# Kernel tuning notes

Hardware: AMD Instinct MI355X
Metric: run time of the kernel (lower is better)

## Reference

```python
import jax, jax.numpy as jnp
import numpy as np

HIDDEN = 1024
ATTN = 512


def setup_inputs() -> dict:
    key = jax.random.key(0)
    ks = jax.random.split(key, 7)
    B, S = 8, 2048
    inputs = jax.random.normal(ks[0], (B, S, HIDDEN), dtype=jnp.float32)
    s = 1.0 / np.sqrt(HIDDEN)
    Wq = jax.random.uniform(ks[1], (HIDDEN, ATTN), jnp.float32, -s, s)
    bq = jax.random.uniform(ks[2], (ATTN,), jnp.float32, -s, s)
    Wk = jax.random.uniform(ks[3], (HIDDEN, ATTN), jnp.float32, -s, s)
    bk = jax.random.uniform(ks[4], (ATTN,), jnp.float32, -s, s)
    Wv = jax.random.uniform(ks[5], (HIDDEN, ATTN), jnp.float32, -s, s)
    bv = jax.random.uniform(ks[6], (ATTN,), jnp.float32, -s, s)
    return {"inputs": inputs, "Wq": Wq, "bq": bq, "Wk": Wk, "bk": bk, "Wv": Wv, "bv": bv}


def reference(inputs, Wq, bq, Wk, bk, Wv, bv):
    # tanh-gated Q/K/V projections
    q = jnp.tanh(inputs @ Wq + bq)        # [B, S, A]
    k = jnp.tanh(inputs @ Wk + bk)        # [B, S, A]
    v = jnp.tanh(inputs @ Wv + bv)        # [B, S, A]
    scores = jnp.einsum('bqa,bka->bqk', q, k) / jnp.sqrt(jnp.float32(ATTN))
    probs = jax.nn.softmax(scores, axis=-1)   # [B, S, S]
    context = jnp.einsum('bqk,bka->bqa', probs, v)
    return jnp.tanh(context), probs
```

## Files before the change

kernel.cpp:

```cpp
#include <hip/hip_runtime.h>
#include <hip/hip_fp16.h>
#include <cstdint>

#define HIDDEN 1024
#define ATTN   512
#define NB     8
#define SEQ    2048
#define MROWS  (NB*SEQ)

typedef _Float16 f16x8 __attribute__((ext_vector_type(8)));
typedef _Float16 f16x4 __attribute__((ext_vector_type(4)));
typedef float    f32x4 __attribute__((ext_vector_type(4)));


__device__ __forceinline__ float tanh_fast(float x){
  float e = __expf(2.0f*x);
  return 1.0f - 2.0f/(e + 1.0f);
}

__device__ __forceinline__ void gload16(const void* g, void* l){
  __builtin_amdgcn_global_load_lds((const __attribute__((address_space(1))) void*)g,
                                   (__attribute__((address_space(3))) void*)l, 16, 0, 0);
}

__global__ __launch_bounds__(256) void k_cast_x(const float* __restrict__ x, __half* __restrict__ xh){
  size_t i = (size_t)blockIdx.x*256 + threadIdx.x;
  const float4* src = reinterpret_cast<const float4*>(x) + i*2;
  float4 a = src[0], b = src[1];
  f16x8 h;
  h[0]=(_Float16)a.x; h[1]=(_Float16)a.y; h[2]=(_Float16)a.z; h[3]=(_Float16)a.w;
  h[4]=(_Float16)b.x; h[5]=(_Float16)b.y; h[6]=(_Float16)b.z; h[7]=(_Float16)b.w;
  reinterpret_cast<f16x8*>(xh)[i] = h;
}

__global__ __launch_bounds__(256) void k_transpose_w(const float* __restrict__ Wq, const float* __restrict__ Wk,
                                                     const float* __restrict__ Wv, __half* __restrict__ whT){
  __shared__ float lds[32][33];
  int which = blockIdx.y;
  const float* W = which==0 ? Wq : (which==1 ? Wk : Wv);
  int tr = blockIdx.x >> 4;
  int tc = blockIdx.x & 15;
  int t = threadIdx.x;
  {
    int r = t >> 3, c4 = (t & 7)*4;
    float4 v = *reinterpret_cast<const float4*>(W + (size_t)(tr*32 + r)*ATTN + tc*32 + c4);
    lds[r][c4+0]=v.x; lds[r][c4+1]=v.y; lds[r][c4+2]=v.z; lds[r][c4+3]=v.w;
  }
  __syncthreads();
  {
    int n = t >> 3, k4 = (t & 7)*4;
    ushort4 u;
    u.x = __half_as_ushort(__float2half(lds[k4+0][n]));
    u.y = __half_as_ushort(__float2half(lds[k4+1][n]));
    u.z = __half_as_ushort(__float2half(lds[k4+2][n]));
    u.w = __half_as_ushort(__float2half(lds[k4+3][n]));
    *reinterpret_cast<ushort4*>(whT + (size_t)which*ATTN*HIDDEN + (size_t)(tc*32 + n)*HIDDEN + tr*32 + k4) = u;
  }
}

__global__ __launch_bounds__(256,3) void k_proj(const __half* __restrict__ xh, const __half* __restrict__ whT,
                                                const float* __restrict__ bq, const float* __restrict__ bk,
                                                const float* __restrict__ bv,
                                                __half* __restrict__ qh, __half* __restrict__ kh, __half* __restrict__ vT){
  __shared__ __align__(16) _Float16 lA[128*64];
  __shared__ __align__(16) _Float16 lB[128*64];
  int nt = blockIdx.x;
  int m0 = blockIdx.y * 128;
  int which = nt >> 2;
  int ncol0 = (nt & 3) * 128;
  int t = threadIdx.x;
  int w = t >> 6, lane = t & 63;
  int lrow = lane & 15, lk = lane >> 4;
  int wm = w >> 1, wn = w & 1;

  int rr = lane >> 3;
  int ss = (lane & 7) ^ rr;
  const __half* Abase = xh + (size_t)(m0 + w*32 + rr)*HIDDEN + ss*8;
  const __half* Bbase = whT + (size_t)which*ATTN*HIDDEN + (size_t)(ncol0 + w*32 + rr)*HIDDEN + ss*8;
  _Float16* lAw = &lA[(w*32)*64];
  _Float16* lBw = &lB[(w*32)*64];

  f32x4 acc[4][4];
  #pragma unroll
  for (int i=0;i<4;i++)
    #pragma unroll
    for (int j=0;j<4;j++) acc[i][j] = f32x4{0.f,0.f,0.f,0.f};

  for (int k0 = 0; k0 < HIDDEN; k0 += 64){
    __syncthreads();
    #pragma unroll
    for (int c=0; c<4; c++){
      gload16(Abase + (size_t)c*8*HIDDEN + k0, &lAw[c*8*64]);
      gload16(Bbase + (size_t)c*8*HIDDEN + k0, &lBw[c*8*64]);
    }
    __syncthreads();
    #pragma unroll
    for (int u=0; u<2; u++){
      f16x8 af[4], bf[4];
      #pragma unroll
      for (int fm=0; fm<4; fm++){
        int row = wm*64 + fm*16 + lrow;
        af[fm] = *(const f16x8*)&lA[row*64 + (((u*4 + lk) ^ (row & 7))*8)];
      }
      #pragma unroll
      for (int fn=0; fn<4; fn++){
        int row = wn*64 + fn*16 + lrow;
        bf[fn] = *(const f16x8*)&lB[row*64 + (((u*4 + lk) ^ (row & 7))*8)];
      }
      #pragma unroll
      for (int fm=0; fm<4; fm++)
        #pragma unroll
        for (int fn=0; fn<4; fn++)
          acc[fm][fn] = __builtin_amdgcn_mfma_f32_16x16x32_f16(af[fm], bf[fn], acc[fm][fn], 0,0,0);
    }
  }

  const float* bias = which==0 ? bq : (which==1 ? bk : bv);
  if (which < 2){
    __half* dst = which==0 ? qh : kh;
    int rt_base = (m0 >> 4) + wm*4;
    int at_base = (ncol0 >> 5) + wn*2;
    #pragma unroll
    for (int fn=0; fn<4; fn++){
      int col = ncol0 + wn*64 + fn*16 + lrow;
      float bb = bias[col];
      int at = at_base + (fn >> 1);
      int asub = (fn & 1)*16 + lrow;
      #pragma unroll
      for (int fm=0; fm<4; fm++){
        size_t tbase = (size_t)(rt_base + fm)*8192 + (size_t)at*512 + asub;
        #pragma unroll
        for (int mi=0; mi<4; mi++)
          dst[tbase + (lk*4 + mi)*32] = __float2half(tanh_fast(acc[fm][fn][mi] + bb));
      }
    }
  } else {
    __half* vb = vT + (size_t)(m0 >> 11)*ATTN*SEQ;
    int jb0 = (m0 & 2047) + wm*64;
    int at0 = (ncol0 >> 4) + wn*4;
    #pragma unroll
    for (int fn=0; fn<4; fn++){
      int col = ncol0 + wn*64 + fn*16 + lrow;
      float bb = bias[col];
      #pragma unroll
      for (int fm=0; fm<4; fm++){
        int jb = jb0 + fm*16;
        f16x4 h;
        #pragma unroll
        for (int mi=0; mi<4; mi++) h[mi] = (_Float16)tanh_fast(acc[fm][fn][mi] + bb);
        *(f16x4*)(vb + (size_t)(at0 + fn)*32768 + (size_t)(jb >> 5)*512 + lrow*32 + (jb & 16) + lk*4) = h;
      }
    }
  }
}

__global__ __launch_bounds__(512,2) void k_scoresE(const __half* __restrict__ qh, const __half* __restrict__ kh,
                                                   __half* __restrict__ p16, float* __restrict__ rsumg){
  __shared__ __align__(16) _Float16 qlds[4*16*512];
  __shared__ __align__(16) _Float16 khlds[64*512];
  __shared__ float partial[8][64];
  int bid = blockIdx.x;
  int b  = bid & 7;
  int i0 = (bid >> 3) * 64;
  int t = threadIdx.x;
  int w = t >> 6, lane = t & 63;
  int lrow = lane & 15, lk = lane >> 4;

  const __half* qsrc = qh + (size_t)((b*SEQ + i0) >> 4)*8192;
  const __half* ksrc = kh + (size_t)b*SEQ*ATTN;
  __half* pb = p16 + (size_t)b*SEQ*SEQ;

  #pragma unroll
  for (int r=0; r<8; r++){
    int chunk = r*8 + w;
    gload16(qsrc + (size_t)chunk*512 + lane*8, &qlds[chunk*512]);
  }

  const float scale = 0.044194173824159216f;
  float esum[4] = {0.f,0.f,0.f,0.f};

  for (int ko = 0; ko < 4; ko++){
    f32x4 acc[4][4];
    #pragma unroll
    for (int i=0;i<4;i++)
      #pragma unroll
      for (int j=0;j<4;j++) acc[i][j] = f32x4{0.f,0.f,0.f,0.f};

    for (int it = 0; it < 16; it += 2){
      __syncthreads();
      #pragma unroll
      for (int j=0; j<4; j++){
        int c = w*4 + j;
        gload16(ksrc + (size_t)(ko*32 + c)*8192 + it*512 + lane*8,       &khlds[c*512]);
        gload16(ksrc + (size_t)(ko*32 + c)*8192 + (it+1)*512 + lane*8,   &khlds[(32 + c)*512]);
      }
      __syncthreads();
      #pragma unroll
      for (int half=0; half<2; half++){
        f16x8 kf[4], qf[4];
        #pragma unroll
        for (int j=0;j<4;j++) kf[j] = *(const f16x8*)&khlds[(half*32 + w*4+j)*512 + lrow*32 + lk*8];
        #pragma unroll
        for (int j=0;j<4;j++) qf[j] = *(const f16x8*)&qlds[(j*16 + it + half)*512 + lrow*32 + lk*8];
        #pragma unroll
        for (int fn=0; fn<4; fn++)
          #pragma unroll
          for (int qi=0; qi<4; qi++)
            acc[qi][fn] = __builtin_amdgcn_mfma_f32_16x16x32_f16(kf[fn], qf[qi], acc[qi][fn], 0,0,0);
      }
    }

    #pragma unroll
    for (int qi=0; qi<4; qi++){
      size_t tq = (size_t)((i0 >> 4) + qi)*32768;
      #pragma unroll
      for (int fn=0; fn<4; fn++){
        f16x4 h;
        float s = 0.f;
        #pragma unroll
        for (int mi=0; mi<4; mi++){
          float e = __expf(acc[qi][fn][mi]*scale);
          h[mi] = (_Float16)e;
          s += e;
        }
        esum[qi] += s;
        *(f16x4*)&pb[tq + (size_t)(ko*16 + w*2 + (fn>>1))*512 + lrow*32 + (fn&1)*16 + lk*4] = h;
      }
    }
  }

  #pragma unroll
  for (int qi=0; qi<4; qi++){
    esum[qi] += __shfl_xor(esum[qi], 16);
    esum[qi] += __shfl_xor(esum[qi], 32);
  }
  if (lane < 16){
    #pragma unroll
    for (int qi=0; qi<4; qi++) partial[w][qi*16 + lane] = esum[qi];
  }
  __syncthreads();
  if (t < 64){
    float s = 0.f;
    #pragma unroll
    for (int ww=0; ww<8; ww++) s += partial[ww][t];
    rsumg[(size_t)b*SEQ + i0 + t] = s;
  }
}

__global__ __launch_bounds__(256,4) void k_expand(const __half* __restrict__ p16, const float* __restrict__ rsumg,
                                                  float* __restrict__ probs){
  __shared__ __align__(16) _Float16 lds[16*2048];
  __shared__ float rs[16];
  int bid = blockIdx.x;
  int b  = bid & 7;
  int tq = bid >> 3;
  int t = threadIdx.x;
  int w = t >> 6, lane = t & 63;

  const __half* src = p16 + (size_t)b*SEQ*SEQ + (size_t)tq*32768;
  #pragma unroll
  for (int i=0; i<16; i++){
    int chunk = i*4 + w;
    gload16(src + (size_t)chunk*512 + lane*8, &lds[chunk*512]);
  }
  if (t < 16) rs[t] = rsumg[(size_t)b*SEQ + tq*16 + t];
  __syncthreads();

  float* pbase = probs + ((size_t)b*SEQ + tq*16)*SEQ;
  #pragma unroll
  for (int rr=0; rr<4; rr++){
    int r = rr*4 + w;
    float iv = 1.0f / rs[r];
    float* prow = pbase + (size_t)r*SEQ;
    #pragma unroll
    for (int ki=0; ki<8; ki++){
      int c = ki*256 + lane*4;
      f16x4 v = *(const f16x4*)&lds[(c >> 5)*512 + r*32 + (c & 31)];
      f32x4 o = {(float)v[0]*iv, (float)v[1]*iv, (float)v[2]*iv, (float)v[3]*iv};
      __builtin_nontemporal_store(o, (f32x4*)(prow + c));
    }
  }
}

__global__ __launch_bounds__(1024,4) void k_scores(const __half* __restrict__ qh, const __half* __restrict__ kh,
                                                   float* __restrict__ probs){
  __shared__ float red[16][32];
  int bid = blockIdx.x;
  int b  = bid & 7;
  int i0 = (bid >> 3) * 32;
  int t = threadIdx.x;
  int w = t >> 6, lane = t & 63;
  int lrow = lane & 15, lk = lane >> 4;
  int loff = lrow*32 + lk*8;

  const __half* kbase = kh + (size_t)((b*SEQ + w*128) >> 4)*8192 + loff;
  const __half* qbase = qh + (size_t)((b*SEQ + i0) >> 4)*8192 + loff;

  f32x4 acc[2][8];
  #pragma unroll
  for (int i=0;i<2;i++)
    #pragma unroll
    for (int j=0;j<8;j++) acc[i][j] = f32x4{0.f,0.f,0.f,0.f};

  for (int it = 0; it < 16; it++){
    f16x8 aq0 = *(const f16x8*)(qbase + it*512);
    f16x8 aq1 = *(const f16x8*)(qbase + 8192 + it*512);
    #pragma unroll
    for (int fn=0; fn<8; fn++){
      f16x8 kf = *(const f16x8*)(kbase + (size_t)fn*8192 + it*512);
      acc[0][fn] = __builtin_amdgcn_mfma_f32_16x16x32_f16(kf, aq0, acc[0][fn], 0,0,0);
      acc[1][fn] = __builtin_amdgcn_mfma_f32_16x16x32_f16(kf, aq1, acc[1][fn], 0,0,0);
    }
  }

  const float scale = 0.044194173824159216f;
  float sm[2];
  #pragma unroll
  for (int nf=0;nf<2;nf++){
    float s = 0.f;
    #pragma unroll
    for (int fn=0;fn<8;fn++)
      #pragma unroll
      for (int mi=0;mi<4;mi++){
        float e = __expf(acc[nf][fn][mi] * scale);
        acc[nf][fn][mi] = e;
        s += e;
      }
    s += __shfl_xor(s, 16);
    s += __shfl_xor(s, 32);
    sm[nf] = s;
  }
  if (lane < 16){ red[w][lane] = sm[0]; red[w][16 + lane] = sm[1]; }
  __syncthreads();
  float inv[2];
  #pragma unroll
  for (int nf=0;nf<2;nf++){
    float tot = 0.f;
    #pragma unroll
    for (int ww=0; ww<16; ww++) tot += red[ww][nf*16 + lrow];
    inv[nf] = 1.0f / tot;
  }
  #pragma unroll
  for (int nf=0;nf<2;nf++){
    f32x4 iv = {inv[nf], inv[nf], inv[nf], inv[nf]};
    #pragma unroll
    for (int fn=0;fn<8;fn++){
      f32x4 v = acc[nf][fn] * iv;
      size_t rowoff = (size_t)(i0 + nf*16 + lrow)*SEQ + w*128 + lk*4;
      *(f32x4*)(probs + (size_t)b*SEQ*SEQ + rowoff + fn*16) = v;
    }
  }
}

__global__ __launch_bounds__(512,4) void k_pv_p16(const __half* __restrict__ p16, const __half* __restrict__ vT,
                                                  const float* __restrict__ rsumg, float* __restrict__ out0){
  int bid = blockIdx.x;
  int b  = bid & 7;
  int i0 = (bid >> 3) * 64;
  int t = threadIdx.x;
  int w = t >> 6, lane = t & 63;
  int lrow = lane & 15, lk = lane >> 4;
  int loff = lrow*32 + lk*8;

  const __half* pbase = p16 + (size_t)b*SEQ*SEQ + (size_t)(i0 >> 4)*32768 + loff;
  const __half* vbase = vT + (size_t)b*ATTN*SEQ + (size_t)(w*4)*32768 + loff;

  f32x4 acc[4][4];
  #pragma unroll
  for (int i=0;i<4;i++)
    #pragma unroll
    for (int j=0;j<4;j++) acc[i][j] = f32x4{0.f,0.f,0.f,0.f};

  for (int kt = 0; kt < 64; kt++){
    f16x8 pa[4];
    #pragma unroll
    for (int nf=0; nf<4; nf++)
      pa[nf] = *(const f16x8*)(pbase + (size_t)nf*32768 + kt*512);
    #pragma unroll
    for (int cf=0; cf<4; cf++){
      f16x8 bv8 = *(const f16x8*)(vbase + (size_t)cf*32768 + kt*512);
      #pragma unroll
      for (int nf=0; nf<4; nf++)
        acc[nf][cf] = __builtin_amdgcn_mfma_f32_16x16x32_f16(pa[nf], bv8, acc[nf][cf], 0,0,0);
    }
  }

  float* dst = out0 + ((size_t)b*SEQ + i0)*ATTN + w*64;
  #pragma unroll
  for (int nf=0; nf<4; nf++){
    f32x4 rs4 = *(const f32x4*)&rsumg[(size_t)b*SEQ + i0 + nf*16 + lk*4];
    #pragma unroll
    for (int mi=0; mi<4; mi++){
      float iv = 1.0f / rs4[mi];
      #pragma unroll
      for (int cf=0; cf<4; cf++)
        __builtin_nontemporal_store(tanh_fast(acc[nf][cf][mi]*iv),
                                    dst + (size_t)(nf*16 + lk*4 + mi)*ATTN + cf*16 + lrow);
    }
  }
}

__global__ __launch_bounds__(512,4) void k_pv(const float* __restrict__ probs, const __half* __restrict__ vT,
                                              float* __restrict__ out0){
  int bid = blockIdx.x;
  int b  = bid & 7;
  int i0 = (bid >> 3) * 32;
  int t = threadIdx.x;
  int w = t >> 6, lane = t & 63;
  int lrow = lane & 15, lk = lane >> 4;
  int loff = lrow*32 + lk*8;

  const float* pbase = probs + ((size_t)b*SEQ + i0 + lrow)*SEQ + lk*8;
  const __half* vbase = vT + (size_t)b*ATTN*SEQ + (size_t)(w*4)*32768 + loff;

  f32x4 acc[2][4];
  #pragma unroll
  for (int i=0;i<2;i++)
    #pragma unroll
    for (int j=0;j<4;j++) acc[i][j] = f32x4{0.f,0.f,0.f,0.f};

  for (int kt = 0; kt < 64; kt++){
    int k0 = kt*32;
    f16x8 af[2];
    #pragma unroll
    for (int nf=0; nf<2; nf++){
      const float* pr = pbase + (size_t)nf*16*SEQ + k0;
      float4 a = *(const float4*)(pr);
      float4 c = *(const float4*)(pr + 4);
      f16x8 h;
      h[0]=(_Float16)a.x; h[1]=(_Float16)a.y; h[2]=(_Float16)a.z; h[3]=(_Float16)a.w;
      h[4]=(_Float16)c.x; h[5]=(_Float16)c.y; h[6]=(_Float16)c.z; h[7]=(_Float16)c.w;
      af[nf] = h;
    }
    #pragma unroll
    for (int cf=0; cf<4; cf++){
      f16x8 bv8 = *(const f16x8*)(vbase + (size_t)cf*32768 + kt*512);
      acc[0][cf] = __builtin_amdgcn_mfma_f32_16x16x32_f16(af[0], bv8, acc[0][cf], 0,0,0);
      acc[1][cf] = __builtin_amdgcn_mfma_f32_16x16x32_f16(af[1], bv8, acc[1][cf], 0,0,0);
    }
  }

  float* dst = out0 + ((size_t)b*SEQ + i0)*ATTN + w*64;
  #pragma unroll
  for (int nf=0; nf<2; nf++)
    #pragma unroll
    for (int cf=0; cf<4; cf++)
      #pragma unroll
      for (int mi=0; mi<4; mi++)
        dst[(size_t)(nf*16 + lk*4 + mi)*ATTN + cf*16 + lrow] = tanh_fast(acc[nf][cf][mi]);
}

extern "C" void kernel_launch(void* const* d_in, const int* in_sizes, int n_in,
                              void* d_out, int out_size, void* d_ws, size_t ws_size,
                              hipStream_t stream){
  const float* x  = (const float*)d_in[0];
  const float* Wq = (const float*)d_in[1];
  const float* bq = (const float*)d_in[2];
  const float* Wk = (const float*)d_in[3];
  const float* bk = (const float*)d_in[4];
  const float* Wv = (const float*)d_in[5];
  const float* bv = (const float*)d_in[6];

  float* out0 = (float*)d_out;
  float* out1 = out0 + (size_t)NB*SEQ*ATTN;

  const size_t SZ = 16777216;
  char* ws = (char*)d_ws;

  if (ws_size >= 5*SZ + 65536){
    __half* vT    = (__half*)ws;
    __half* p16   = (__half*)(ws + SZ);
    float*  rsumg = (float*)(ws + 5*SZ);
    __half* xh  = (__half*)out1;
    __half* whT = (__half*)((char*)out1 + 2*SZ);
    __half* qh  = (__half*)((char*)out1 + 2*SZ + 3145728);
    __half* kh  = (__half*)((char*)out1 + 3*SZ + 3145728);
    k_cast_x     <<<8192,        256, 0, stream>>>(x, xh);
    k_transpose_w<<<dim3(512,3), 256, 0, stream>>>(Wq, Wk, Wv, whT);
    k_proj       <<<dim3(12,128),256, 0, stream>>>(xh, whT, bq, bk, bv, qh, kh, vT);
    k_scoresE    <<<256,         512, 0, stream>>>(qh, kh, p16, rsumg);
    k_expand     <<<1024,        256, 0, stream>>>(p16, rsumg, out1);
    k_pv_p16     <<<256,         512, 0, stream>>>(p16, vT, rsumg, out0);
  } else if (ws_size >= 3*SZ){
    __half* vT = (__half*)ws;
    __half* qh = (__half*)(ws + SZ);
    __half* kh = (__half*)(ws + 2*SZ);
    __half* xh  = (__half*)out1;
    __half* whT = (__half*)((char*)out1 + 2*SZ);
    k_cast_x     <<<8192,        256, 0, stream>>>(x, xh);
    k_transpose_w<<<dim3(512,3), 256, 0, stream>>>(Wq, Wk, Wv, whT);
    k_proj       <<<dim3(12,128),256, 0, stream>>>(xh, whT, bq, bk, bv, qh, kh, vT);
    k_scores     <<<512,        1024, 0, stream>>>(qh, kh, out1);
    k_pv         <<<512,         512, 0, stream>>>(out1, vT, out0);
  } else {
    __half* vT = (__half*)ws;
    __half* qh = (__half*)out0;
    __half* kh = (__half*)out0 + (size_t)MROWS*ATTN;
    __half* xh  = (__half*)out1;
    __half* whT = (__half*)((char*)out1 + 2*SZ);
    k_cast_x     <<<8192,        256, 0, stream>>>(x, xh);
    k_transpose_w<<<dim3(512,3), 256, 0, stream>>>(Wq, Wk, Wv, whT);
    k_proj       <<<dim3(12,128),256, 0, stream>>>(xh, whT, bq, bk, bv, qh, kh, vT);
    k_scores     <<<512,        1024, 0, stream>>>(qh, kh, out1);
    k_pv         <<<512,         512, 0, stream>>>(out1, vT, out0);
  }
}
```

Baseline: 266.5 us.

## Fuse probs expansion into scores kernel when workspace is large enough

Adds a new path that writes normalized fp32 probabilities directly from k_scoresE after the row sums are reduced, dropping the separate k_expand launch. Q and K move into workspace so the probs output buffer is not aliased while it is being written. The fused epilogue re-reads the just-written fp16 p16 tile from global memory, which may still be cache-resident, and the kernel now carries a large store tail at 2 blocks per CU. This only runs if the workspace is at least 7*16MB plus 64KB.

After: 273.7 us. +2.7%, slower.

```diff
diff --git a/kernel.cpp b/kernel.cpp
--- a/kernel.cpp
+++ b/kernel.cpp
@@ -155,10 +155,12 @@
 }
 
 __global__ __launch_bounds__(512,2) void k_scoresE(const __half* __restrict__ qh, const __half* __restrict__ kh,
-                                                   __half* __restrict__ p16, float* __restrict__ rsumg){
+                                                   __half* __restrict__ p16, float* __restrict__ rsumg,
+                                                   float* __restrict__ probs){
   __shared__ __align__(16) _Float16 qlds[4*16*512];
   __shared__ __align__(16) _Float16 khlds[64*512];
   __shared__ float partial[8][64];
+  __shared__ float rs64[64];
   int bid = blockIdx.x;
   int b  = bid & 7;
   int i0 = (bid >> 3) * 64;
@@ -244,6 +246,28 @@
     #pragma unroll
     for (int ww=0; ww<8; ww++) s += partial[ww][t];
     rsumg[(size_t)b*SEQ + i0 + t] = s;
+    rs64[t] = s;
+  }
+  __syncthreads();
+
+  if (probs){
+    float* pr0 = probs + ((size_t)b*SEQ + i0)*SEQ;
+    #pragma unroll
+    for (int rr2=0; rr2<8; rr2++){
+      int r = w*8 + rr2;
+      float iv = 1.0f / rs64[r];
+      const __half* src = pb + (size_t)((i0 >> 4) + (r >> 4))*32768 + (r & 15)*32;
+      float* prow = pr0 + (size_t)r*SEQ;
+      #pragma unroll
+      for (int ki=0; ki<4; ki++){
+        int c = ki*512 + lane*8;
+        f16x8 v = *(const f16x8*)(src + (size_t)(c >> 5)*512 + (c & 31));
+        f32x4 lo = {(float)v[0]*iv, (float)v[1]*iv, (float)v[2]*iv, (float)v[3]*iv};
+        f32x4 hi = {(float)v[4]*iv, (float)v[5]*iv, (float)v[6]*iv, (float)v[7]*iv};
+        __builtin_nontemporal_store(lo, (f32x4*)(prow + c));
+        __builtin_nontemporal_store(hi, (f32x4*)(prow + c + 4));
+      }
+    }
   }
 }
 
@@ -282,6 +306,54 @@
   }
 }
 
+__global__ __launch_bounds__(512,4) void k_pv_p16(const __half* __restrict__ p16, const __half* __restrict__ vT,
+                                                  const float* __restrict__ rsumg, float* __restrict__ out0){
+  int bid = blockIdx.x;
+  int b  = bid & 7;
+  int i0 = (bid >> 3) * 64;
+  int t = threadIdx.x;
+  int w = t >> 6, lane = t & 63;
+  int lrow = lane & 15, lk = lane >> 4;
+  int loff = lrow*32 + lk*8;
+
+  const __half* pbase = p16 + (size_t)b*SEQ*SEQ + (size_t)(i0 >> 4)*32768 + loff;
+  const __half* vbase = vT + (size_t)b*ATTN*SEQ + (size_t)(w*4)*32768 + loff;
+
+  f32x4 acc[4][4];
+  #pragma unroll
+  for (int i=0;i<4;i++)
+    #pragma unroll
+    for (int j=0;j<4;j++) acc[i][j] = f32x4{0.f,0.f,0.f,0.f};
+
+  for (int kt = 0; kt < 64; kt++){
+    f16x8 pa[4];
+    #pragma unroll
+    for (int nf=0; nf<4; nf++)
+      pa[nf] = *(const f16x8*)(pbase + (size_t)nf*32768 + kt*512);
+    #pragma unroll
+    for (int cf=0; cf<4; cf++){
+      f16x8 bv8 = *(const f16x8*)(vbase + (size_t)cf*32768 + kt*512);
+      #pragma unroll
+      for (int nf=0; nf<4; nf++)
+        acc[nf][cf] = __builtin_amdgcn_mfma_f32_16x16x32_f16(pa[nf], bv8, acc[nf][cf], 0,0,0);
+    }
+  }
+
+  float* dst = out0 + ((size_t)b*SEQ + i0)*ATTN + w*64;
+  #pragma unroll
+  for (int nf=0; nf<4; nf++){
+    f32x4 rs4 = *(const f32x4*)&rsumg[(size_t)b*SEQ + i0 + nf*16 + lk*4];
+    #pragma unroll
+    for (int mi=0; mi<4; mi++){
+      float iv = 1.0f / rs4[mi];
+      #pragma unroll
+      for (int cf=0; cf<4; cf++)
+        __builtin_nontemporal_store(tanh_fast(acc[nf][cf][mi]*iv),
+                                    dst + (size_t)(nf*16 + lk*4 + mi)*ATTN + cf*16 + lrow);
+    }
+  }
+}
+
 __global__ __launch_bounds__(1024,4) void k_scores(const __half* __restrict__ qh, const __half* __restrict__ kh,
                                                    float* __restrict__ probs){
   __shared__ float red[16][32];
@@ -348,54 +420,6 @@
       f32x4 v = acc[nf][fn] * iv;
       size_t rowoff = (size_t)(i0 + nf*16 + lrow)*SEQ + w*128 + lk*4;
       *(f32x4*)(probs + (size_t)b*SEQ*SEQ + rowoff + fn*16) = v;
-    }
-  }
-}
-
-__global__ __launch_bounds__(512,4) void k_pv_p16(const __half* __restrict__ p16, const __half* __restrict__ vT,
-                                                  const float* __restrict__ rsumg, float* __restrict__ out0){
-  int bid = blockIdx.x;
-  int b  = bid & 7;
-  int i0 = (bid >> 3) * 64;
-  int t = threadIdx.x;
-  int w = t >> 6, lane = t & 63;
-  int lrow = lane & 15, lk = lane >> 4;
-  int loff = lrow*32 + lk*8;
-
-  const __half* pbase = p16 + (size_t)b*SEQ*SEQ + (size_t)(i0 >> 4)*32768 + loff;
-  const __half* vbase = vT + (size_t)b*ATTN*SEQ + (size_t)(w*4)*32768 + loff;
-
-  f32x4 acc[4][4];
-  #pragma unroll
-  for (int i=0;i<4;i++)
-    #pragma unroll
-    for (int j=0;j<4;j++) acc[i][j] = f32x4{0.f,0.f,0.f,0.f};
-
-  for (int kt = 0; kt < 64; kt++){
-    f16x8 pa[4];
-    #pragma unroll
-    for (int nf=0; nf<4; nf++)
-      pa[nf] = *(const f16x8*)(pbase + (size_t)nf*32768 + kt*512);
-    #pragma unroll
-    for (int cf=0; cf<4; cf++){
-      f16x8 bv8 = *(const f16x8*)(vbase + (size_t)cf*32768 + kt*512);
-      #pragma unroll
-      for (int nf=0; nf<4; nf++)
-        acc[nf][cf] = __builtin_amdgcn_mfma_f32_16x16x32_f16(pa[nf], bv8, acc[nf][cf], 0,0,0);
-    }
-  }
-
-  float* dst = out0 + ((size_t)b*SEQ + i0)*ATTN + w*64;
-  #pragma unroll
-  for (int nf=0; nf<4; nf++){
-    f32x4 rs4 = *(const f32x4*)&rsumg[(size_t)b*SEQ + i0 + nf*16 + lk*4];
-    #pragma unroll
-    for (int mi=0; mi<4; mi++){
-      float iv = 1.0f / rs4[mi];
-      #pragma unroll
-      for (int cf=0; cf<4; cf++)
-        __builtin_nontemporal_store(tanh_fast(acc[nf][cf][mi]*iv),
-                                    dst + (size_t)(nf*16 + lk*4 + mi)*ATTN + cf*16 + lrow);
     }
   }
 }
@@ -467,7 +491,20 @@
   const size_t SZ = 16777216;
   char* ws = (char*)d_ws;
 
-  if (ws_size >= 5*SZ + 65536){
+  if (ws_size >= 7*SZ + 65536){
+    __half* vT    = (__half*)ws;
+    __half* p16   = (__half*)(ws + SZ);
+    float*  rsumg = (float*)(ws + 5*SZ);
+    __half* qh    = (__half*)(ws + 5*SZ + 65536);
+    __half* kh    = (__half*)(ws + 6*SZ + 65536);
+    __half* xh  = (__half*)out1;
+    __half* whT = (__half*)((char*)out1 + 2*SZ);
+    k_cast_x     <<<8192,        256, 0, stream>>>(x, xh);
+    k_transpose_w<<<dim3(512,3), 256, 0, stream>>>(Wq, Wk, Wv, whT);
+    k_proj       <<<dim3(12,128),256, 0, stream>>>(xh, whT, bq, bk, bv, qh, kh, vT);
+    k_scoresE    <<<256,         512, 0, stream>>>(qh, kh, p16, rsumg, out1);
+    k_pv_p16     <<<256,         512, 0, stream>>>(p16, vT, rsumg, out0);
+  } else if (ws_size >= 5*SZ + 65536){
     __half* vT    = (__half*)ws;
     __half* p16   = (__half*)(ws + SZ);
     float*  rsumg = (float*)(ws + 5*SZ);
@@ -478,7 +515,7 @@
     k_cast_x     <<<8192,        256, 0, stream>>>(x, xh);
     k_transpose_w<<<dim3(512,3), 256, 0, stream>>>(Wq, Wk, Wv, whT);
     k_proj       <<<dim3(12,128),256, 0, stream>>>(xh, whT, bq, bk, bv, qh, kh, vT);
-    k_scoresE    <<<256,         512, 0, stream>>>(qh, kh, p16, rsumg);
+    k_scoresE    <<<256,         512, 0, stream>>>(qh, kh, p16, rsumg, (float*)nullptr);
     k_expand     <<<1024,        256, 0, stream>>>(p16, rsumg, out1);
     k_pv_p16     <<<256,         512, 0, stream>>>(p16, vT, rsumg, out0);
   } else if (ws_size >= 3*SZ){
```
